# Kernel tuning notes

Measured on AMD Instinct MI355X. Metric: run time of the kernel, lower is better.

The kernel has to match this reference:

```python
import jax, jax.numpy as jnp
import numpy as np

I = 256  # input size
H = 256  # hidden size
B = 128
S = 1024
EPS = 1e-5


def setup_inputs() -> dict:
    key = jax.random.key(0)
    ks = jax.random.split(key, 8)
    bound = 1.0 / np.sqrt(H)
    x = jax.random.normal(ks[0], (B, S, I), dtype=jnp.float32)
    mask = jax.random.randint(ks[1], (B, S), 0, 2) == 1
    W_ih = jax.random.uniform(ks[2], (4 * H, I), jnp.float32, -bound, bound)
    W_hh = jax.random.uniform(ks[3], (4 * H, H), jnp.float32, -bound, bound)
    b_ih = jax.random.uniform(ks[4], (4 * H,), jnp.float32, -bound, bound)
    b_hh = jax.random.uniform(ks[5], (4 * H,), jnp.float32, -bound, bound)
    gamma = jnp.ones((H,), jnp.float32)
    beta = jnp.zeros((H,), jnp.float32)
    return {"x": x, "mask": mask, "W_ih": W_ih, "W_hh": W_hh,
            "b_ih": b_ih, "b_hh": b_hh, "gamma": gamma, "beta": beta}


def _layernorm(h, gamma, beta):
    mu = jnp.mean(h, axis=-1, keepdims=True)
    var = jnp.var(h, axis=-1, keepdims=True)
    return (h - mu) * jax.lax.rsqrt(var + EPS) * gamma + beta


def reference(x, mask, W_ih, W_hh, b_ih, b_hh, gamma, beta):
    b = x.shape[0]
    h0 = jnp.zeros((b, H), x.dtype)
    c0 = jnp.zeros((b, H), x.dtype)
    out0 = jnp.zeros((b, H), x.dtype)

    def step(carry, inp):
        h, c, out = carry
        x_t, m_t = inp  # (B,I), (B,)
        hn = _layernorm(h, gamma, beta)
        gates = x_t @ W_ih.T + b_ih + hn @ W_hh.T + b_hh  # (B,4H)
        i_g, f_g, g_g, o_g = jnp.split(gates, 4, axis=-1)
        c = jax.nn.sigmoid(f_g) * c + jax.nn.sigmoid(i_g) * jnp.tanh(g_g)
        h = jax.nn.sigmoid(o_g) * jnp.tanh(c)
        # output[~mask] = h[~mask]; where mask is True the old output is kept
        out = jnp.where(m_t[:, None], out, h)
        return (h, c, out), None

    xs = (jnp.swapaxes(x, 0, 1), jnp.swapaxes(mask, 0, 1))  # (S,B,I), (S,B)
    (h, c, out), _ = jax.lax.scan(step, (h0, c0, out0), xs)
    return out
```

## Files before the change

kernel.cpp:

```cpp
#include <hip/hip_runtime.h>
#include <hip/hip_bf16.h>
#include <stdint.h>


#define Bb 128
#define Ss 1024
#define Ii 256
#define Hh 256
#define G4v 1024
#define EPSF 1e-5f

typedef __bf16 bf16;
typedef _Float16 f16;
typedef __attribute__((ext_vector_type(8))) __bf16 bf16x8;
typedef __attribute__((ext_vector_type(4))) _Float16 f16x4;
typedef __attribute__((ext_vector_type(8))) _Float16 f16x8;
typedef __attribute__((ext_vector_type(4))) float f32x4;
typedef unsigned int u32;
typedef unsigned long long u64;

static __device__ __forceinline__ f32x4 mfma16b(bf16x8 a, bf16x8 b, f32x4 c) {
  return __builtin_amdgcn_mfma_f32_16x16x32_bf16(a, b, c, 0, 0, 0);
}
static __device__ __forceinline__ f32x4 mfma16h(f16x8 a, f16x8 b, f32x4 c) {
  return __builtin_amdgcn_mfma_f32_16x16x32_f16(a, b, c, 0, 0, 0);
}
static __device__ __forceinline__ float sigm(float x) { return 1.0f / (1.0f + __expf(-x)); }
static __device__ __forceinline__ float tanhf_(float x) {
  float e = __expf(-2.0f * fabsf(x));
  float t = (1.0f - e) / (1.0f + e);
  return x < 0.0f ? -t : t;
}
static __device__ __forceinline__ unsigned short ush(f16 h) {
  return __builtin_bit_cast(unsigned short, h);
}
static __device__ __forceinline__ f16 hus(unsigned short u) {
  return __builtin_bit_cast(f16, u);
}

__global__ void k_conv_wih(const float* __restrict__ W, bf16* __restrict__ hi,
                           bf16* __restrict__ lo) {
  int i = (blockIdx.x * 256 + threadIdx.x) * 4;
  f32x4 v = *(const f32x4*)(W + i);
#pragma unroll
  for (int j = 0; j < 4; ++j) {
    bf16 hh = (bf16)v[j];
    hi[i + j] = hh;
    lo[i + j] = (bf16)(v[j] - (float)hh);
  }
}

__global__ void k_prep_whh(const float* __restrict__ W, const float* __restrict__ gamma,
                           f16* __restrict__ Wf) {
  int tid = blockIdx.x * 256 + threadIdx.x;
  int lane = tid & 63;
  int fk = tid >> 6;
  int ntg = fk >> 3, kt = fk & 7;
  int g = ntg * 16 + (lane & 15);
  int k = kt * 32 + ((lane >> 4) << 3);
  f16x8 r;
#pragma unroll
  for (int j = 0; j < 8; ++j) r[j] = (f16)(W[g * Hh + k + j] * gamma[k + j]);
  *(f16x8*)(Wf + (size_t)tid * 8) = r;
}

__global__ void k_prep_rd(const float* __restrict__ W, const float* __restrict__ gamma,
                          const float* __restrict__ beta, const float* __restrict__ bih,
                          const float* __restrict__ bhh, float* __restrict__ RD) {
  int g = blockIdx.x * 256 + threadIdx.x;
  float r = 0.f, d = 0.f;
  for (int k = 0; k < Hh; ++k) {
    float w = W[g * Hh + k];
    r += w * gamma[k];
    d += w * beta[k];
  }
  RD[2 * g] = r;
  RD[2 * g + 1] = d + bih[g] + bhh[g];
}

__global__ __launch_bounds__(256, 2) void k_gemm(const float* __restrict__ x,
                                                 const bf16* __restrict__ Whi,
                                                 const bf16* __restrict__ Wlo,
                                                 float* __restrict__ xw,
                                                 int t0, int Tc, int ntb) {
  __shared__ bf16 Bs[2][128 * 128];
  int bid = blockIdx.x;
  int b = bid & 127;
  int r2 = bid >> 7;
  int tb = r2 % ntb;
  int gt = r2 / ntb;
  int g0 = gt * 128;
  int tid = threadIdx.x, w = tid >> 6, lane = tid & 63;
  int li = lane & 15, lg = lane >> 4;
  char* BsB = (char*)Bs;
  int tbase = tb * 128 + 32 * w;
  f32x4 acc[2][8];
#pragma unroll
  for (int mt = 0; mt < 2; ++mt)
#pragma unroll
    for (int nt = 0; nt < 8; ++nt) acc[mt][nt] = (f32x4){0.f, 0.f, 0.f, 0.f};

  for (int kp = 0; kp < 2; ++kp) {
#pragma unroll
    for (int it = 0; it < 8; ++it) {
      int p = it * 4096 + tid * 16;
      int row = p >> 8, colb = p & 255;
      size_t goff = (size_t)(g0 + row) * 512 + kp * 256 + colb;
      int dst = row * 256 + (colb ^ ((row & 7) << 4));
      *(bf16x8*)(BsB + dst) = *(const bf16x8*)((const char*)Whi + goff);
      *(bf16x8*)(BsB + 32768 + dst) = *(const bf16x8*)((const char*)Wlo + goff);
    }
    __syncthreads();
#pragma unroll
    for (int kt = 0; kt < 4; ++kt) {
      int kl = kt * 32 + lg * 8;
      int kgl = kp * 128 + kl;
      bf16x8 ah[2], al[2];
#pragma unroll
      for (int mt = 0; mt < 2; ++mt) {
        int t = t0 + tbase + 16 * mt + li;
        const float* xp = x + ((size_t)b * Ss + t) * Ii + kgl;
        f32x4 f0 = *(const f32x4*)xp;
        f32x4 f1 = *(const f32x4*)(xp + 4);
        bf16x8 hv, lv;
#pragma unroll
        for (int j = 0; j < 4; ++j) {
          bf16 h0 = (bf16)f0[j];
          hv[j] = h0;
          lv[j] = (bf16)(f0[j] - (float)h0);
          bf16 h1 = (bf16)f1[j];
          hv[4 + j] = h1;
          lv[4 + j] = (bf16)(f1[j] - (float)h1);
        }
        ah[mt] = hv;
        al[mt] = lv;
      }
#pragma unroll
      for (int nt = 0; nt < 8; ++nt) {
        int grow = nt * 16 + li;
        int off = grow * 256 + ((kl * 2) ^ ((grow & 7) << 4));
        bf16x8 bh = *(const bf16x8*)(BsB + off);
        bf16x8 bl = *(const bf16x8*)(BsB + 32768 + off);
#pragma unroll
        for (int mt = 0; mt < 2; ++mt) {
          acc[mt][nt] = mfma16b(ah[mt], bh, acc[mt][nt]);
          acc[mt][nt] = mfma16b(ah[mt], bl, acc[mt][nt]);
          acc[mt][nt] = mfma16b(al[mt], bh, acc[mt][nt]);
        }
      }
    }
    __syncthreads();
  }
#pragma unroll
  for (int mt = 0; mt < 2; ++mt)
#pragma unroll
    for (int nt = 0; nt < 8; ++nt)
#pragma unroll
      for (int r = 0; r < 4; ++r) {
        int tl = tbase + 16 * mt + lg * 4 + r;
        int g = g0 + nt * 16 + li;
        xw[((size_t)b * Tc + tl) * G4v + g] = acc[mt][nt][r];
      }
}

__global__ __launch_bounds__(256, 1) void k_recur(
    const f16* __restrict__ Wf, const float* __restrict__ xw,
    const int* __restrict__ mask, const float* __restrict__ RD,
    float* __restrict__ st_h, float* __restrict__ st_c, float* __restrict__ st_o,
    u64* pub, float* __restrict__ out, int t0, int Tc, int first, int last) {
  __shared__ f16 hbH[16 * 256];
  __shared__ f16 hbL[16 * 256];
  __shared__ float murs[2][16][2];
  __shared__ float2 spw[4][16];
  __shared__ float spart[16][16][2];
  int bid = blockIdx.x;
  int grp = bid & 7, q = bid >> 3;
  int tid = threadIdx.x, w = tid >> 6, lane = tid & 63;
  int li = lane & 15, lg = lane >> 4;
  int b0 = grp * 16;
  int jloc = (q * 4 + w) * 16 + li;
  char* hbHB = (char*)hbH;
  char* hbLB = (char*)hbL;

  f16x8 wp[4][8];
#pragma unroll
  for (int c = 0; c < 4; ++c)
#pragma unroll
    for (int kt = 0; kt < 8; ++kt) {
      int ntg = c * 16 + q * 4 + w;
      wp[c][kt] = *(const f16x8*)(Wf + ((size_t)(ntg * 8 + kt) * 64 + lane) * 8);
      asm volatile("" : "+a"(wp[c][kt]));
    }
  float Rr[4], Dd[4];
#pragma unroll
  for (int c = 0; c < 4; ++c) {
    int g = c * 256 + jloc;
    Rr[c] = RD[2 * g];
    Dd[c] = RD[2 * g + 1];
  }

  float cst[4], ost[4];
  if (first) {
#pragma unroll
    for (int i = 0; i < 16; ++i) {
      hbH[tid * 16 + i] = (f16)0.0f;
      hbL[tid * 16 + i] = (f16)0.0f;
    }
#pragma unroll
    for (int r = 0; r < 4; ++r) { cst[r] = 0.f; ost[r] = 0.f; }
    if (tid < 16) { murs[0][tid][0] = 0.f; murs[0][tid][1] = rsqrtf(EPSF); }
  } else {
    int row = tid >> 4, cs = tid & 15, jseg = cs * 16;
    float s = 0.f, ss = 0.f;
#pragma unroll
    for (int i = 0; i < 16; ++i) {
      float v = st_h[(size_t)(b0 + row) * Hh + jseg + i];
      s += v;
      ss += v * v;
      f16 hh = (f16)v;
      int boff = row * 512 + (((jseg + i) * 2) ^ ((row & 7) << 4));
      *(f16*)(hbHB + boff) = hh;
      *(f16*)(hbLB + boff) = (f16)(v - (float)hh);
    }
    spart[row][cs][0] = s;
    spart[row][cs][1] = ss;
#pragma unroll
    for (int r = 0; r < 4; ++r) {
      int m = lg * 4 + r;
      cst[r] = st_c[(size_t)(b0 + m) * Hh + jloc];
      ost[r] = st_o[(size_t)(b0 + m) * Hh + jloc];
    }
    __syncthreads();
    if (tid < 16) {
      float s2 = 0.f, ss2 = 0.f;
#pragma unroll
      for (int i = 0; i < 16; ++i) { s2 += spart[tid][i][0]; ss2 += spart[tid][i][1]; }
      float mu = s2 * (1.f / 256.f);
      float var = ss2 * (1.f / 256.f) - mu * mu;
      float rs = rsqrtf(var + EPSF);
      murs[0][tid][0] = mu * rs;
      murs[0][tid][1] = rs;
    }
  }
  __syncthreads();

  float xwv[4][4];
  int mk[4];
#pragma unroll
  for (int c = 0; c < 4; ++c)
#pragma unroll
    for (int r = 0; r < 4; ++r)
      xwv[c][r] = xw[((size_t)(b0 + lg * 4 + r) * Tc + 0) * G4v + c * 256 + jloc];
#pragma unroll
  for (int r = 0; r < 4; ++r) mk[r] = mask[(size_t)(b0 + lg * 4 + r) * Ss + t0];

  int grow = tid >> 4, gcg = tid & 15;

  for (int tl = 0; tl < Tc; ++tl) {
    int tg = t0 + tl;
    int slot = (tg + 1) & 1;
    u32 want = (u32)(tg + 1);

    f32x4 a0[4], a1[4];
#pragma unroll
    for (int c = 0; c < 4; ++c) {
      a0[c] = (f32x4){0.f, 0.f, 0.f, 0.f};
      a1[c] = (f32x4){0.f, 0.f, 0.f, 0.f};
    }
#pragma unroll
    for (int kt = 0; kt < 8; ++kt) {
      int aoff = li * 512 + (((kt * 32 + lg * 8) * 2) ^ ((li & 7) << 4));
      f16x8 ah = *(const f16x8*)(hbHB + aoff);
      f16x8 al = *(const f16x8*)(hbLB + aoff);
#pragma unroll
      for (int c = 0; c < 4; ++c) {
        a0[c] = mfma16h(ah, wp[c][kt], a0[c]);
        a1[c] = mfma16h(al, wp[c][kt], a1[c]);
      }
    }
    float mrs[4], rsv[4];
#pragma unroll
    for (int r = 0; r < 4; ++r) {
      int m = lg * 4 + r;
      mrs[r] = murs[tl & 1][m][0];
      rsv[r] = murs[tl & 1][m][1];
    }
    __syncthreads();

    float hnew[4];
#pragma unroll
    for (int r = 0; r < 4; ++r) {
      float i_ = (a0[0][r] + a1[0][r]) * rsv[r] - mrs[r] * Rr[0] + Dd[0] + xwv[0][r];
      float f_ = (a0[1][r] + a1[1][r]) * rsv[r] - mrs[r] * Rr[1] + Dd[1] + xwv[1][r];
      float g_ = (a0[2][r] + a1[2][r]) * rsv[r] - mrs[r] * Rr[2] + Dd[2] + xwv[2][r];
      float o_ = (a0[3][r] + a1[3][r]) * rsv[r] - mrs[r] * Rr[3] + Dd[3] + xwv[3][r];
      float cn = sigm(f_) * cst[r] + sigm(i_) * tanhf_(g_);
      float hn = sigm(o_) * tanhf_(cn);
      cst[r] = cn;
      ost[r] = mk[r] ? ost[r] : hn;
      hnew[r] = hn;
      int m = lg * 4 + r;
      f16 hh = (f16)hn;
      int boff = m * 512 + ((jloc * 2) ^ ((m & 7) << 4));
      *(f16*)(hbHB + boff) = hh;
      *(f16*)(hbLB + boff) = (f16)(hn - (float)hh);
    }
    {
      u64* ph = pub + (size_t)(slot * 32 + bid) * 512;
#pragma unroll
      for (int r = 0; r < 4; ++r) {
        float ho = __shfl_xor(hnew[r], 1);
        if (!(li & 1)) {
          u64 pv = ((u64)want << 32) | ((u32)ush((f16)hnew[r]) << 16) |
                   (u32)ush((f16)ho);
          __hip_atomic_store(&ph[(lg * 4 + r) * 32 + w * 8 + (li >> 1)], pv,
                             __ATOMIC_RELAXED, __HIP_MEMORY_SCOPE_AGENT);
        }
      }
    }

    u64 gv[3][2];
    const u64* srcs[3];
#pragma unroll
    for (int pi = 0; pi < 3; ++pi) {
      int qq = (q + 1 + pi) & 3;
      int pbid = qq * 8 + grp;
      srcs[pi] = pub + (size_t)(slot * 32 + pbid) * 512 + grow * 32 + gcg * 2;
      gv[pi][0] = __hip_atomic_load(&srcs[pi][0], __ATOMIC_RELAXED,
                                    __HIP_MEMORY_SCOPE_AGENT);
      gv[pi][1] = __hip_atomic_load(&srcs[pi][1], __ATOMIC_RELAXED,
                                    __HIP_MEMORY_SCOPE_AGENT);
    }

    {
      float sr[4], qr[4];
#pragma unroll
      for (int r = 0; r < 4; ++r) { sr[r] = hnew[r]; qr[r] = hnew[r] * hnew[r]; }
#pragma unroll
      for (int msk = 1; msk < 16; msk <<= 1)
#pragma unroll
        for (int r = 0; r < 4; ++r) {
          sr[r] += __shfl_xor(sr[r], msk);
          qr[r] += __shfl_xor(qr[r], msk);
        }
      if (li == 0)
#pragma unroll
        for (int r = 0; r < 4; ++r) spw[w][lg * 4 + r] = make_float2(sr[r], qr[r]);
    }
    if (tl == Tc - 1) {
#pragma unroll
      for (int r = 0; r < 4; ++r) {
        int m = lg * 4 + r;
        st_h[(size_t)(b0 + m) * Hh + jloc] = hnew[r];
        st_c[(size_t)(b0 + m) * Hh + jloc] = cst[r];
        st_o[(size_t)(b0 + m) * Hh + jloc] = ost[r];
      }
      if (last) {
#pragma unroll
        for (int r = 0; r < 4; ++r) out[(size_t)(b0 + lg * 4 + r) * Hh + jloc] = ost[r];
      }
    }
    {
      int tln = (tl + 1 < Tc) ? tl + 1 : Tc - 1;
#pragma unroll
      for (int c = 0; c < 4; ++c)
#pragma unroll
        for (int r = 0; r < 4; ++r)
          xwv[c][r] = xw[((size_t)(b0 + lg * 4 + r) * Tc + tln) * G4v + c * 256 + jloc];
#pragma unroll
      for (int r = 0; r < 4; ++r) mk[r] = mask[(size_t)(b0 + lg * 4 + r) * Ss + t0 + tln];
    }

    {
      u32 bad = 0;
#pragma unroll
      for (int pi = 0; pi < 3; ++pi)
#pragma unroll
        for (int e = 0; e < 2; ++e) bad |= (u32)(gv[pi][e] >> 32) ^ want;
      int cnt = 0;
      while (bad) {
#pragma unroll
        for (int pi = 0; pi < 3; ++pi)
#pragma unroll
          for (int e = 0; e < 2; ++e)
            gv[pi][e] = __hip_atomic_load(&srcs[pi][e], __ATOMIC_RELAXED,
                                          __HIP_MEMORY_SCOPE_AGENT);
        bad = 0;
#pragma unroll
        for (int pi = 0; pi < 3; ++pi)
#pragma unroll
          for (int e = 0; e < 2; ++e) bad |= (u32)(gv[pi][e] >> 32) ^ want;
        if (++cnt > (1 << 20)) break;
      }
    }
    float su = 0.f, qu = 0.f;
#pragma unroll
    for (int pi = 0; pi < 3; ++pi) {
      int qq = (q + 1 + pi) & 3;
      int j0 = qq * 64 + gcg * 4;
      int boff = grow * 512 + ((j0 * 2) ^ ((grow & 7) << 4));
      u32 d0 = (u32)gv[pi][0], d1 = (u32)gv[pi][1];
      f16x4 h4;
      h4[0] = hus((unsigned short)(d0 >> 16));
      h4[1] = hus((unsigned short)(d0 & 0xffffu));
      h4[2] = hus((unsigned short)(d1 >> 16));
      h4[3] = hus((unsigned short)(d1 & 0xffffu));
      f16x4 z4 = (f16x4){(f16)0.f, (f16)0.f, (f16)0.f, (f16)0.f};
      *(f16x4*)(hbHB + boff) = h4;
      *(f16x4*)(hbLB + boff) = z4;
#pragma unroll
      for (int e = 0; e < 4; ++e) {
        float f = (float)h4[e];
        su += f;
        qu += f * f;
      }
    }
#pragma unroll
    for (int msk = 1; msk < 16; msk <<= 1) {
      su += __shfl_xor(su, msk);
      qu += __shfl_xor(qu, msk);
    }
    __syncthreads();
    if (li == 0) {
      float s = su + spw[0][grow].x + spw[1][grow].x + spw[2][grow].x + spw[3][grow].x;
      float ss2 = qu + spw[0][grow].y + spw[1][grow].y + spw[2][grow].y + spw[3][grow].y;
      float mu = s * (1.f / 256.f);
      float var = ss2 * (1.f / 256.f) - mu * mu;
      float rs = rsqrtf(var + EPSF);
      murs[(tl + 1) & 1][grow][0] = mu * rs;
      murs[(tl + 1) & 1][grow][1] = rs;
    }
    __syncthreads();
  }
}

extern "C" void kernel_launch(void* const* d_in, const int* in_sizes, int n_in,
                              void* d_out, int out_size, void* d_ws, size_t ws_size,
                              hipStream_t stream) {
  (void)in_sizes; (void)n_in; (void)out_size;
  const float* x = (const float*)d_in[0];
  const int* mask = (const int*)d_in[1];
  const float* Wih = (const float*)d_in[2];
  const float* Whh = (const float*)d_in[3];
  const float* bih = (const float*)d_in[4];
  const float* bhh = (const float*)d_in[5];
  const float* gamma = (const float*)d_in[6];
  const float* beta = (const float*)d_in[7];
  float* outp = (float*)d_out;
  char* ws = (char*)d_ws;

  const size_t extra = 3 * (512u << 10) + (8u << 10) + 3 * (128u << 10) +
                       (256u << 10) + (64u << 10);
  int Tc = 128;
  if (ws_size >= (size_t)1024 * 524288 + extra) Tc = 1024;
  else if (ws_size >= (size_t)512 * 524288 + extra) Tc = 512;
  else if (ws_size >= (size_t)256 * 524288 + extra) Tc = 256;

  size_t o = 0;
  auto take = [&](size_t bytes) { size_t r = o; o += (bytes + 255) & ~(size_t)255; return r; };
  size_t xw_off = take((size_t)Bb * Tc * G4v * 4);
  size_t wihh_off = take(512u << 10);
  size_t wihl_off = take(512u << 10);
  size_t whh_off = take(512u << 10);
  size_t rd_off = take(8u << 10);
  size_t sth_off = take(128u << 10);
  size_t stc_off = take(128u << 10);
  size_t sto_off = take(128u << 10);
  size_t pub_off = take(256u << 10);

  bf16* wihh = (bf16*)(ws + wihh_off);
  bf16* wihl = (bf16*)(ws + wihl_off);
  f16* whhf = (f16*)(ws + whh_off);
  float* rd = (float*)(ws + rd_off);
  float* xwp = (float*)(ws + xw_off);
  float* sth = (float*)(ws + sth_off);
  float* stc = (float*)(ws + stc_off);
  float* sto = (float*)(ws + sto_off);
  u64* pubh = (u64*)(ws + pub_off);

  hipMemsetAsync(pubh, 0, 256u << 10, stream);
  k_conv_wih<<<dim3(256), dim3(256), 0, stream>>>(Wih, wihh, wihl);
  k_prep_whh<<<dim3(128), dim3(256), 0, stream>>>(Whh, gamma, whhf);
  k_prep_rd<<<dim3(4), dim3(256), 0, stream>>>(Whh, gamma, beta, bih, bhh, rd);

  int nchunk = Ss / Tc;
  int ntb = Tc / 128;
  for (int ci = 0; ci < nchunk; ++ci) {
    int t0 = ci * Tc;
    k_gemm<<<dim3(8 * ntb * 128), dim3(256), 0, stream>>>(x, wihh, wihl, xwp, t0, Tc, ntb);
    k_recur<<<dim3(32), dim3(256), 0, stream>>>(whhf, xwp, mask, rd, sth, stc, sto,
                                                pubh, outp, t0, Tc,
                                                ci == 0 ? 1 : 0, ci == nchunk - 1 ? 1 : 0);
  }
}
```

Baseline: 3.868 ms.

## Pack four f16 hidden values per flag word using LSB parity as sequence tag

```diff
diff --git a/kernel.cpp b/kernel.cpp
--- a/kernel.cpp
+++ b/kernel.cpp
@@ -255,11 +255,14 @@
   for (int r = 0; r < 4; ++r) mk[r] = mask[(size_t)(b0 + lg * 4 + r) * Ss + t0];
 
   int grow = tid >> 4, gcg = tid & 15;
+  int bq = li & 3;
+  const u64 PMASK = 0x0001000100010001ull;
 
   for (int tl = 0; tl < Tc; ++tl) {
     int tg = t0 + tl;
     int slot = (tg + 1) & 1;
-    u32 want = (u32)(tg + 1);
+    u32 wpar = ((u32)(tg + 1) >> 1) & 1;
+    u64 wantp = wpar ? PMASK : 0;
 
     f32x4 a0[4], a1[4];
 #pragma unroll
@@ -306,30 +309,45 @@
       *(f16*)(hbLB + boff) = (f16)(hn - (float)hh);
     }
     {
-      u64* ph = pub + (size_t)(slot * 32 + bid) * 512;
-#pragma unroll
-      for (int r = 0; r < 4; ++r) {
-        float ho = __shfl_xor(hnew[r], 1);
-        if (!(li & 1)) {
-          u64 pv = ((u64)want << 32) | ((u32)ush((f16)hnew[r]) << 16) |
-                   (u32)ush((f16)ho);
-          __hip_atomic_store(&ph[(lg * 4 + r) * 32 + w * 8 + (li >> 1)], pv,
-                             __ATOMIC_RELAXED, __HIP_MEMORY_SCOPE_AGENT);
-        }
-      }
-    }
-
-    u64 gv[3][2];
+      float tp[4];
+#pragma unroll
+      for (int r = 0; r < 4; ++r) tp[r] = hnew[r];
+      {
+        float s01 = (bq & 1) ? tp[0] : tp[1];
+        float r01 = __shfl_xor(s01, 1);
+        if (bq & 1) tp[0] = r01; else tp[1] = r01;
+        float s23 = (bq & 1) ? tp[2] : tp[3];
+        float r23 = __shfl_xor(s23, 1);
+        if (bq & 1) tp[2] = r23; else tp[3] = r23;
+        float s02 = (bq & 2) ? tp[0] : tp[2];
+        float r02 = __shfl_xor(s02, 2);
+        if (bq & 2) tp[0] = r02; else tp[2] = r02;
+        float s13 = (bq & 2) ? tp[1] : tp[3];
+        float r13 = __shfl_xor(s13, 2);
+        if (bq & 2) tp[1] = r13; else tp[3] = r13;
+      }
+      u64 pv = 0;
+#pragma unroll
+      for (int a = 0; a < 4; ++a) {
+        u32 hw = (u32)ush((f16)tp[a]);
+        hw = (hw & ~1u) | wpar;
+        pv |= (u64)hw << (16 * a);
+      }
+      u64* ph = pub + (size_t)(slot * 32 + bid) * 256;
+      int m2 = lg * 4 + bq;
+      int cg = w * 4 + ((li & 12) >> 2);
+      __hip_atomic_store(&ph[m2 * 16 + cg], pv, __ATOMIC_RELAXED,
+                         __HIP_MEMORY_SCOPE_AGENT);
+    }
+
+    u64 gv[3];
     const u64* srcs[3];
 #pragma unroll
     for (int pi = 0; pi < 3; ++pi) {
       int qq = (q + 1 + pi) & 3;
       int pbid = qq * 8 + grp;
-      srcs[pi] = pub + (size_t)(slot * 32 + pbid) * 512 + grow * 32 + gcg * 2;
-      gv[pi][0] = __hip_atomic_load(&srcs[pi][0], __ATOMIC_RELAXED,
-                                    __HIP_MEMORY_SCOPE_AGENT);
-      gv[pi][1] = __hip_atomic_load(&srcs[pi][1], __ATOMIC_RELAXED,
-                                    __HIP_MEMORY_SCOPE_AGENT);
+      srcs[pi] = pub + (size_t)(slot * 32 + pbid) * 256 + grow * 16 + gcg;
+      gv[pi] = __hip_atomic_load(srcs[pi], __ATOMIC_RELAXED, __HIP_MEMORY_SCOPE_AGENT);
     }
 
     {
@@ -374,22 +392,22 @@
     {
       u32 bad = 0;
 #pragma unroll
-      for (int pi = 0; pi < 3; ++pi)
-#pragma unroll
-        for (int e = 0; e < 2; ++e) bad |= (u32)(gv[pi][e] >> 32) ^ want;
+      for (int pi = 0; pi < 3; ++pi) {
+        u64 d = (gv[pi] & PMASK) ^ wantp;
+        bad |= (u32)d | (u32)(d >> 32);
+      }
       int cnt = 0;
       while (bad) {
 #pragma unroll
         for (int pi = 0; pi < 3; ++pi)
-#pragma unroll
-          for (int e = 0; e < 2; ++e)
-            gv[pi][e] = __hip_atomic_load(&srcs[pi][e], __ATOMIC_RELAXED,
-                                          __HIP_MEMORY_SCOPE_AGENT);
+          gv[pi] = __hip_atomic_load(srcs[pi], __ATOMIC_RELAXED,
+                                     __HIP_MEMORY_SCOPE_AGENT);
         bad = 0;
 #pragma unroll
-        for (int pi = 0; pi < 3; ++pi)
-#pragma unroll
-          for (int e = 0; e < 2; ++e) bad |= (u32)(gv[pi][e] >> 32) ^ want;
+        for (int pi = 0; pi < 3; ++pi) {
+          u64 d = (gv[pi] & PMASK) ^ wantp;
+          bad |= (u32)d | (u32)(d >> 32);
+        }
         if (++cnt > (1 << 20)) break;
       }
     }
@@ -399,12 +417,9 @@
       int qq = (q + 1 + pi) & 3;
       int j0 = qq * 64 + gcg * 4;
       int boff = grow * 512 + ((j0 * 2) ^ ((grow & 7) << 4));
-      u32 d0 = (u32)gv[pi][0], d1 = (u32)gv[pi][1];
       f16x4 h4;
-      h4[0] = hus((unsigned short)(d0 >> 16));
-      h4[1] = hus((unsigned short)(d0 & 0xffffu));
-      h4[2] = hus((unsigned short)(d1 >> 16));
-      h4[3] = hus((unsigned short)(d1 & 0xffffu));
+#pragma unroll
+      for (int a = 0; a < 4; ++a) h4[a] = hus((unsigned short)(gv[pi] >> (16 * a)));
       f16x4 z4 = (f16x4){(f16)0.f, (f16)0.f, (f16)0.f, (f16)0.f};
       *(f16x4*)(hbHB + boff) = h4;
       *(f16x4*)(hbLB + boff) = z4;
@@ -478,7 +493,7 @@
   float* sto = (float*)(ws + sto_off);
   u64* pubh = (u64*)(ws + pub_off);
 
-  hipMemsetAsync(pubh, 0, 256u << 10, stream);
+  hipMemsetAsync(pubh, 0x01, 256u << 10, stream);
   k_conv_wih<<<dim3(256), dim3(256), 0, stream>>>(Wih, wihh, wihl);
   k_prep_whh<<<dim3(128), dim3(256), 0, stream>>>(Whh, gamma, whhf);
   k_prep_rd<<<dim3(4), dim3(256), 0, stream>>>(Whh, gamma, beta, bih, bhh, rd);
```

Result: slower. 4.433 ms (+14.6%).
